# Kernel tuning notes

Measured on AMD Instinct MI355X. Metric: run time of the kernel, lower is better.

## Reference

```python
import jax, jax.numpy as jnp
import numpy as np

K = 10          # hardcoded in module (self.K = 10)
H = 26          # neighbors per query point in this run
PAD_H = 28      # layer_ind2neighbor[layer_ind=0]
KP_EXTENT = 1.2 # linear-influence extent


def setup_inputs() -> dict:
    key = jax.random.key(0)
    ks = jax.random.split(key, 6)
    N, Ns, Cin, Cout = 65536, 65536, 64, 128
    q_pts = jax.random.normal(ks[0], (N, 3), jnp.float32)
    s_pts = jax.random.normal(ks[1], (Ns, 3), jnp.float32)
    neighb_inds = jax.random.randint(ks[2], (N, H), 0, Ns)
    x = jax.random.normal(ks[3], (Ns, Cin), jnp.float32)
    # kernel_points_generator: Linear(PAD_H*3 -> K*3)
    gen_W = jax.random.normal(ks[4], (K * 3, PAD_H * 3), jnp.float32) * (1.0 / np.sqrt(PAD_H * 3))
    gen_b = jnp.zeros((K * 3,), jnp.float32)
    # KPConv weights: [K, in, out] (kaiming_uniform in torch; scaled normal here)
    weights = jax.random.normal(ks[5], (K, Cin, Cout), jnp.float32) * (1.0 / np.sqrt(Cin))
    return {"q_pts": q_pts, "s_pts": s_pts, "x": x,
            "gen_W": gen_W, "gen_b": gen_b, "weights": weights,
            "neighb_inds": neighb_inds}


def _kpconv(q_pts, s_pts, x, gen_W, gen_b, weights, neighb_inds):
    N = q_pts.shape[0]
    # shadow support point far away (index Ns)
    s_pad = jnp.concatenate([s_pts, jnp.full((1, 3), 1e6, s_pts.dtype)], axis=0)
    neighbors = s_pad[neighb_inds] - q_pts[:, None, :]                          # [N,H,3]
    # generative kernel points: pad neighbor list with -1 up to PAD_H, run linear
    padded = jnp.concatenate(
        [neighbors, jnp.full((N, PAD_H - H, 3), -1.0, neighbors.dtype)], axis=1)
    kp = (padded.reshape(N, -1) @ gen_W.T + gen_b).reshape(N, 1, K, 3)          # [N,1,K,3]
    diff = neighbors[:, :, None, :] - kp                                        # [N,H,K,3]
    sq_d = jnp.sum(diff * diff, axis=3)                                         # [N,H,K]
    # KP_influence == 'linear'
    all_w = jnp.maximum(1.0 - jnp.sqrt(sq_d) / KP_EXTENT, 0.0)
    all_w = jnp.swapaxes(all_w, 1, 2)                                           # [N,K,H]
    # shadow feature row (zeros) at index Ns
    x_pad = jnp.concatenate([x, jnp.zeros((1, x.shape[1]), x.dtype)], axis=0)
    neighb_x = x_pad[neighb_inds]                                               # [N,H,Cin]
    weighted = jnp.einsum('nkh,nhi->nki', all_w, neighb_x)                      # [N,K,Cin]
    return jnp.einsum('nki,kio->no', weighted, weights)                         # [N,Cout]


def reference(q_pts, s_pts, x, gen_W, gen_b, weights, neighb_inds):
    return _kpconv(q_pts, s_pts, x, gen_W, gen_b, weights, neighb_inds)
```

## Files before the change

kernel.cpp:

```cpp
#include <hip/hip_runtime.h>
#include <stdint.h>

#define N_Q   65536
#define N_S   65536
#define NB_H  26
#define PAD_H 28
#define KP    10
#define CIN   64
#define COUT  128
#define MT    8
#define BM    16
#define NPASS (BM / MT)

typedef unsigned short u16x8  __attribute__((ext_vector_type(8)));
typedef float          f32x4  __attribute__((ext_vector_type(4)));
typedef _Float16       f16x8  __attribute__((ext_vector_type(8)));
typedef _Float16       f16x2  __attribute__((ext_vector_type(2)));

#define CVT_BLOCKS 2049
#define PACK_BLOCKS 40

static __device__ __forceinline__ unsigned short f2h(float f) {
  return __builtin_bit_cast(unsigned short, (_Float16)f);
}

static __device__ __forceinline__ unsigned int pkrtz_u32(float a, float b) {
  return __builtin_bit_cast(unsigned int, __builtin_amdgcn_cvt_pkrtz(a, b));
}

static __device__ __forceinline__ float fdot2u(unsigned int a, unsigned int b, float c) {
#if __has_builtin(__builtin_amdgcn_fdot2)
  return __builtin_amdgcn_fdot2(__builtin_bit_cast(f16x2, a),
                                __builtin_bit_cast(f16x2, b), c, false);
#else
  f16x2 ha = __builtin_bit_cast(f16x2, a), hb = __builtin_bit_cast(f16x2, b);
  return c + (float)ha[0] * (float)hb[0] + (float)ha[1] * (float)hb[1];
#endif
}

__global__ void prep_kernel(const float* __restrict__ x,
                            const float* __restrict__ w,
                            unsigned short* __restrict__ xh,
                            unsigned short* __restrict__ bp) {
  if (blockIdx.x < CVT_BLOCKS) {
    long t = (long)blockIdx.x * blockDim.x + threadIdx.x;
    long off = t * 8;
    if (off >= (long)(N_S + 1) * CIN) return;
    u16x8 o;
    if (off < (long)N_S * CIN) {
      f32x4 a = *(const f32x4*)(x + off);
      f32x4 b = *(const f32x4*)(x + off + 4);
      o[0] = f2h(a[0]); o[1] = f2h(a[1]); o[2] = f2h(a[2]); o[3] = f2h(a[3]);
      o[4] = f2h(b[0]); o[5] = f2h(b[1]); o[6] = f2h(b[2]); o[7] = f2h(b[3]);
    } else {
      o = (u16x8)0;
    }
    *(u16x8*)(xh + off) = o;
  } else {
    int t = (blockIdx.x - CVT_BLOCKS) * blockDim.x + threadIdx.x;
    if (t >= 8 * 20 * 64) return;
    int lane = t & 63;
    int frag = t >> 6;
    int ks = frag % 20;
    int ct = frag / 20;
    int row0 = ks * 32 + (lane >> 4) * 8;
    int col  = ct * 16 + (lane & 15);
    u16x8 o;
    #pragma unroll
    for (int j = 0; j < 8; ++j) o[j] = f2h(w[(row0 + j) * COUT + col]);
    *(u16x8*)(bp + (long)t * 8) = o;
  }
}

__global__ void __launch_bounds__(256, 5)
kpconv_fused(const float* __restrict__ q_pts, const float* __restrict__ s_pts,
             const float* __restrict__ gen_W, const float* __restrict__ gen_b,
             const int* __restrict__ inds, const unsigned short* __restrict__ xh,
             const unsigned short* __restrict__ bp, float* __restrict__ out) {

  __shared__ int            sh_ind[MT][NB_H];
  __shared__ float          sh_nbr[MT][80];
  __shared__ float          sh_kp[MT][KP * 3];
  __shared__ unsigned int   sh_aw[MT][13][12];
  __shared__ unsigned short sA[20 * 512];

  const int  tid  = threadIdx.x;
  const long row0 = (long)blockIdx.x * BM;

  #pragma unroll 1
  for (int pass = 0; pass < NPASS; ++pass) {
    const int pbase = (int)row0 + pass * MT;

    if (tid < MT * NB_H) {
      int m = tid / NB_H, h = tid % NB_H;
      int n = pbase + m;
      int ind = inds[n * NB_H + h];
      sh_ind[m][h] = ind;
      float sx, sy, sz;
      if ((unsigned)ind < (unsigned)N_S) {
        sx = s_pts[ind * 3 + 0]; sy = s_pts[ind * 3 + 1]; sz = s_pts[ind * 3 + 2];
      } else {
        sx = 1e6f; sy = 1e6f; sz = 1e6f;
      }
      sh_nbr[m][h * 3 + 0] = sx - q_pts[n * 3 + 0];
      sh_nbr[m][h * 3 + 1] = sy - q_pts[n * 3 + 1];
      sh_nbr[m][h * 3 + 2] = sz - q_pts[n * 3 + 2];
    }
    if (tid < MT * 2) sh_nbr[tid >> 1][78 + (tid & 1)] = -1.0f;
    __syncthreads();

    if (tid < MT * KP * 3) {
      int m = tid / 30, r = tid % 30;
      const float* Wr = gen_W + r * (PAD_H * 3);
      const f32x4* W4 = (const f32x4*)Wr;
      const f32x4* N4 = (const f32x4*)&sh_nbr[m][0];
      f32x4 accv = {0.f, 0.f, 0.f, 0.f};
      #pragma unroll
      for (int j = 0; j < 20; ++j) accv += W4[j] * N4[j];
      sh_kp[m][r] = gen_b[r] - (Wr[80] + Wr[81] + Wr[82] + Wr[83])
                  + accv[0] + accv[1] + accv[2] + accv[3];
    }
    __syncthreads();

    for (int p = tid; p < MT * 13 * KP; p += 256) {
      int k = p % KP;
      int t = p / KP;
      int m = t & (MT - 1);
      int hp = t >> 3;
      float kx = sh_kp[m][k * 3 + 0], ky = sh_kp[m][k * 3 + 1], kz = sh_kp[m][k * 3 + 2];
      int h0 = hp * 2;
      float dx0 = sh_nbr[m][h0 * 3 + 0] - kx;
      float dy0 = sh_nbr[m][h0 * 3 + 1] - ky;
      float dz0 = sh_nbr[m][h0 * 3 + 2] - kz;
      float w0 = fmaxf(1.0f - sqrtf(dx0 * dx0 + dy0 * dy0 + dz0 * dz0) * (1.0f / 1.2f), 0.0f);
      float dx1 = sh_nbr[m][h0 * 3 + 3] - kx;
      float dy1 = sh_nbr[m][h0 * 3 + 4] - ky;
      float dz1 = sh_nbr[m][h0 * 3 + 5] - kz;
      float w1 = fmaxf(1.0f - sqrtf(dx1 * dx1 + dy1 * dy1 + dz1 * dz1) * (1.0f / 1.2f), 0.0f);
      sh_aw[m][hp][k] = pkrtz_u32(w0, w1);
    }
    __syncthreads();

    {
      const int m  = tid >> 5;
      const int i0 = (tid & 31) * 2;
      float acc0[KP], acc1[KP];
      #pragma unroll
      for (int k = 0; k < KP; ++k) { acc0[k] = 0.f; acc1[k] = 0.f; }

      unsigned int xr[8];
      #pragma unroll
      for (int h = 0; h < 8; ++h)
        xr[h] = *(const unsigned int*)(xh + (long)sh_ind[m][h] * CIN + i0);

      #pragma unroll
      for (int p = 0; p < 13; ++p) {
        unsigned int r0 = xr[(2 * p) & 7];
        unsigned int r1 = xr[(2 * p + 1) & 7];
        if (2 * p + 8 < NB_H)
          xr[(2 * p) & 7] = *(const unsigned int*)(xh + (long)sh_ind[m][2 * p + 8] * CIN + i0);
        if (2 * p + 9 < NB_H)
          xr[(2 * p + 1) & 7] = *(const unsigned int*)(xh + (long)sh_ind[m][2 * p + 9] * CIN + i0);
        unsigned int pair0 = __builtin_amdgcn_perm(r1, r0, 0x05040100u);
        unsigned int pair1 = __builtin_amdgcn_perm(r1, r0, 0x07060302u);
        const unsigned int* wrow = &sh_aw[m][p][0];
        #pragma unroll
        for (int k = 0; k < KP; ++k) {
          unsigned int w2 = wrow[k];
          acc0[k] = fdot2u(w2, pair0, acc0[k]);
          acc1[k] = fdot2u(w2, pair1, acc1[k]);
        }
      }
      const int row  = pass * MT + m;
      const int qhi  = i0 >> 5;
      const int e    = i0 & 31;
      const int slot = row * 4 + (e >> 3);
      const int hoff = slot * 8 + (e & 7);
      #pragma unroll
      for (int k = 0; k < KP; ++k)
        *(unsigned int*)(sA + (k * 2 + qhi) * 512 + hoff) = pkrtz_u32(acc0[k], acc1[k]);
    }
    __syncthreads();
  }

  {
    const int wave = tid >> 6;
    const int lane = tid & 63;
    const int ct0  = wave * 2, ct1 = ct0 + 1;
    const int aoff = ((lane & 15) * 4 + (lane >> 4)) * 8;

    f32x4 acc[2];
    acc[0] = (f32x4){0.f, 0.f, 0.f, 0.f};
    acc[1] = (f32x4){0.f, 0.f, 0.f, 0.f};

    u16x8 pb0[4], pb1[4];
    #pragma unroll
    for (int d = 0; d < 4; ++d) {
      pb0[d] = *(const u16x8*)(bp + (long)((ct0 * 20 + d) * 64 + lane) * 8);
      pb1[d] = *(const u16x8*)(bp + (long)((ct1 * 20 + d) * 64 + lane) * 8);
    }

    #pragma unroll
    for (int ks = 0; ks < 20; ++ks) {
      f16x8 b0 = __builtin_bit_cast(f16x8, pb0[ks & 3]);
      f16x8 b1 = __builtin_bit_cast(f16x8, pb1[ks & 3]);
      if (ks + 4 < 20) {
        pb0[ks & 3] = *(const u16x8*)(bp + (long)((ct0 * 20 + ks + 4) * 64 + lane) * 8);
        pb1[ks & 3] = *(const u16x8*)(bp + (long)((ct1 * 20 + ks + 4) * 64 + lane) * 8);
      }
      u16x8 au = *(const u16x8*)&sA[ks * 512 + aoff];
      f16x8 a = __builtin_bit_cast(f16x8, au);
      acc[0] = __builtin_amdgcn_mfma_f32_16x16x32_f16(a, b0, acc[0], 0, 0, 0);
      acc[1] = __builtin_amdgcn_mfma_f32_16x16x32_f16(a, b1, acc[1], 0, 0, 0);
    }

    const int col   = lane & 15;
    const int rbase = (lane >> 4) * 4;
    #pragma unroll
    for (int r = 0; r < 4; ++r) {
      long row = row0 + rbase + r;
      __builtin_nontemporal_store(acc[0][r], &out[row * COUT + ct0 * 16 + col]);
      __builtin_nontemporal_store(acc[1][r], &out[row * COUT + ct1 * 16 + col]);
    }
  }
}

extern "C" void kernel_launch(void* const* d_in, const int* in_sizes, int n_in,
                              void* d_out, int out_size, void* d_ws, size_t ws_size,
                              hipStream_t stream) {
  const float* q_pts = (const float*)d_in[0];
  const float* s_pts = (const float*)d_in[1];
  const float* x     = (const float*)d_in[2];
  const float* gen_W = (const float*)d_in[3];
  const float* gen_b = (const float*)d_in[4];
  const float* wts   = (const float*)d_in[5];
  const int*   inds  = (const int*)d_in[6];
  float* out = (float*)d_out;

  unsigned short* xh = (unsigned short*)d_ws;
  unsigned short* bp = xh + (size_t)(N_S + 1) * CIN;

  prep_kernel<<<CVT_BLOCKS + PACK_BLOCKS, 256, 0, stream>>>(x, wts, xh, bp);
  kpconv_fused<<<N_Q / BM, 256, 0, stream>>>(q_pts, s_pts, gen_W, gen_b,
                                             inds, xh, bp, out);
}
```

Before: 174.1 us.

## Process all 16 rows in one pass with two rows per thread and swizzled LDS

The two 8-row passes are merged into a single 16-row stage, so each thread gathers and accumulates features for two query rows (A and B) at once. This halves the number of block-wide barriers and doubles the independent gather loads in flight per thread. Kernel-weight reads from shared memory become vectorized 16/8-byte loads. The intermediate A-tile layout in shared memory is XOR-swizzled, with the MFMA-side address changed to match, to reduce bank conflicts. In exchange, register and LDS use per block rise, and launch bounds drop from 5 to 4 blocks per CU, lowering occupancy.

Result: no change. 175.7 us (+0.9%).

```diff
diff --git a/kernel.cpp b/kernel.cpp
--- a/kernel.cpp
+++ b/kernel.cpp
@@ -8,14 +8,15 @@
 #define KP    10
 #define CIN   64
 #define COUT  128
-#define MT    8
+#define MT    16
 #define BM    16
-#define NPASS (BM / MT)
 
 typedef unsigned short u16x8  __attribute__((ext_vector_type(8)));
 typedef float          f32x4  __attribute__((ext_vector_type(4)));
 typedef _Float16       f16x8  __attribute__((ext_vector_type(8)));
 typedef _Float16       f16x2  __attribute__((ext_vector_type(2)));
+typedef unsigned int   u32x4  __attribute__((ext_vector_type(4)));
+typedef unsigned int   u32x2  __attribute__((ext_vector_type(2)));
 
 #define CVT_BLOCKS 2049
 #define PACK_BLOCKS 40
@@ -72,7 +73,7 @@
   }
 }
 
-__global__ void __launch_bounds__(256, 5)
+__global__ void __launch_bounds__(256, 4)
 kpconv_fused(const float* __restrict__ q_pts, const float* __restrict__ s_pts,
              const float* __restrict__ gen_W, const float* __restrict__ gen_b,
              const int* __restrict__ inds, const unsigned short* __restrict__ xh,
@@ -87,107 +88,126 @@
   const int  tid  = threadIdx.x;
   const long row0 = (long)blockIdx.x * BM;
 
-  #pragma unroll 1
-  for (int pass = 0; pass < NPASS; ++pass) {
-    const int pbase = (int)row0 + pass * MT;
-
-    if (tid < MT * NB_H) {
-      int m = tid / NB_H, h = tid % NB_H;
-      int n = pbase + m;
-      int ind = inds[n * NB_H + h];
-      sh_ind[m][h] = ind;
-      float sx, sy, sz;
-      if ((unsigned)ind < (unsigned)N_S) {
-        sx = s_pts[ind * 3 + 0]; sy = s_pts[ind * 3 + 1]; sz = s_pts[ind * 3 + 2];
-      } else {
-        sx = 1e6f; sy = 1e6f; sz = 1e6f;
-      }
-      sh_nbr[m][h * 3 + 0] = sx - q_pts[n * 3 + 0];
-      sh_nbr[m][h * 3 + 1] = sy - q_pts[n * 3 + 1];
-      sh_nbr[m][h * 3 + 2] = sz - q_pts[n * 3 + 2];
-    }
-    if (tid < MT * 2) sh_nbr[tid >> 1][78 + (tid & 1)] = -1.0f;
-    __syncthreads();
-
-    if (tid < MT * KP * 3) {
-      int m = tid / 30, r = tid % 30;
-      const float* Wr = gen_W + r * (PAD_H * 3);
-      const f32x4* W4 = (const f32x4*)Wr;
-      const f32x4* N4 = (const f32x4*)&sh_nbr[m][0];
-      f32x4 accv = {0.f, 0.f, 0.f, 0.f};
+  for (int it = tid; it < MT * NB_H; it += 256) {
+    int m = it / NB_H, h = it % NB_H;
+    int n = (int)row0 + m;
+    int ind = inds[n * NB_H + h];
+    sh_ind[m][h] = ind;
+    float sx, sy, sz;
+    if ((unsigned)ind < (unsigned)N_S) {
+      sx = s_pts[ind * 3 + 0]; sy = s_pts[ind * 3 + 1]; sz = s_pts[ind * 3 + 2];
+    } else {
+      sx = 1e6f; sy = 1e6f; sz = 1e6f;
+    }
+    sh_nbr[m][h * 3 + 0] = sx - q_pts[n * 3 + 0];
+    sh_nbr[m][h * 3 + 1] = sy - q_pts[n * 3 + 1];
+    sh_nbr[m][h * 3 + 2] = sz - q_pts[n * 3 + 2];
+  }
+  if (tid < MT * 2) sh_nbr[tid >> 1][78 + (tid & 1)] = -1.0f;
+  __syncthreads();
+
+  for (int it = tid; it < MT * KP * 3; it += 256) {
+    int m = it / 30, r = it % 30;
+    const float* Wr = gen_W + r * (PAD_H * 3);
+    const f32x4* W4 = (const f32x4*)Wr;
+    const f32x4* N4 = (const f32x4*)&sh_nbr[m][0];
+    f32x4 accv = {0.f, 0.f, 0.f, 0.f};
+    #pragma unroll
+    for (int j = 0; j < 20; ++j) accv += W4[j] * N4[j];
+    sh_kp[m][r] = gen_b[r] - (Wr[80] + Wr[81] + Wr[82] + Wr[83])
+                + accv[0] + accv[1] + accv[2] + accv[3];
+  }
+  __syncthreads();
+
+  for (int p = tid; p < MT * 13 * KP; p += 256) {
+    int k = p % KP;
+    int t = p / KP;
+    int m = t & (MT - 1);
+    int hp = t >> 4;
+    float kx = sh_kp[m][k * 3 + 0], ky = sh_kp[m][k * 3 + 1], kz = sh_kp[m][k * 3 + 2];
+    int h0 = hp * 2;
+    float dx0 = sh_nbr[m][h0 * 3 + 0] - kx;
+    float dy0 = sh_nbr[m][h0 * 3 + 1] - ky;
+    float dz0 = sh_nbr[m][h0 * 3 + 2] - kz;
+    float w0 = fmaxf(1.0f - sqrtf(dx0 * dx0 + dy0 * dy0 + dz0 * dz0) * (1.0f / 1.2f), 0.0f);
+    float dx1 = sh_nbr[m][h0 * 3 + 3] - kx;
+    float dy1 = sh_nbr[m][h0 * 3 + 4] - ky;
+    float dz1 = sh_nbr[m][h0 * 3 + 5] - kz;
+    float w1 = fmaxf(1.0f - sqrtf(dx1 * dx1 + dy1 * dy1 + dz1 * dz1) * (1.0f / 1.2f), 0.0f);
+    sh_aw[m][hp][k] = pkrtz_u32(w0, w1);
+  }
+  __syncthreads();
+
+  {
+    const int g  = tid >> 5;
+    const int l  = tid & 31;
+    const int i0 = l * 2;
+    const int rA = g, rB = g + 8;
+
+    float a0A[KP], a1A[KP], a0B[KP], a1B[KP];
+    #pragma unroll
+    for (int k = 0; k < KP; ++k) { a0A[k] = 0.f; a1A[k] = 0.f; a0B[k] = 0.f; a1B[k] = 0.f; }
+
+    unsigned int xrA[8], xrB[8];
+    #pragma unroll
+    for (int h = 0; h < 8; ++h) {
+      xrA[h] = *(const unsigned int*)(xh + (long)sh_ind[rA][h] * CIN + i0);
+      xrB[h] = *(const unsigned int*)(xh + (long)sh_ind[rB][h] * CIN + i0);
+    }
+
+    #pragma unroll
+    for (int p = 0; p < 13; ++p) {
+      unsigned int r0A = xrA[(2 * p) & 7], r1A = xrA[(2 * p + 1) & 7];
+      unsigned int r0B = xrB[(2 * p) & 7], r1B = xrB[(2 * p + 1) & 7];
+      if (2 * p + 8 < NB_H) {
+        xrA[(2 * p) & 7] = *(const unsigned int*)(xh + (long)sh_ind[rA][2 * p + 8] * CIN + i0);
+        xrB[(2 * p) & 7] = *(const unsigned int*)(xh + (long)sh_ind[rB][2 * p + 8] * CIN + i0);
+      }
+      if (2 * p + 9 < NB_H) {
+        xrA[(2 * p + 1) & 7] = *(const unsigned int*)(xh + (long)sh_ind[rA][2 * p + 9] * CIN + i0);
+        xrB[(2 * p + 1) & 7] = *(const unsigned int*)(xh + (long)sh_ind[rB][2 * p + 9] * CIN + i0);
+      }
+      unsigned int p0A = __builtin_amdgcn_perm(r1A, r0A, 0x05040100u);
+      unsigned int p1A = __builtin_amdgcn_perm(r1A, r0A, 0x07060302u);
+      unsigned int p0B = __builtin_amdgcn_perm(r1B, r0B, 0x05040100u);
+      unsigned int p1B = __builtin_amdgcn_perm(r1B, r0B, 0x07060302u);
+
+      unsigned int wA[KP], wB[KP];
+      *(u32x4*)&wA[0] = *(const u32x4*)&sh_aw[rA][p][0];
+      *(u32x4*)&wA[4] = *(const u32x4*)&sh_aw[rA][p][4];
+      *(u32x2*)&wA[8] = *(const u32x2*)&sh_aw[rA][p][8];
+      *(u32x4*)&wB[0] = *(const u32x4*)&sh_aw[rB][p][0];
+      *(u32x4*)&wB[4] = *(const u32x4*)&sh_aw[rB][p][4];
+      *(u32x2*)&wB[8] = *(const u32x2*)&sh_aw[rB][p][8];
+
       #pragma unroll
-      for (int j = 0; j < 20; ++j) accv += W4[j] * N4[j];
-      sh_kp[m][r] = gen_b[r] - (Wr[80] + Wr[81] + Wr[82] + Wr[83])
-                  + accv[0] + accv[1] + accv[2] + accv[3];
-    }
-    __syncthreads();
-
-    for (int p = tid; p < MT * 13 * KP; p += 256) {
-      int k = p % KP;
-      int t = p / KP;
-      int m = t & (MT - 1);
-      int hp = t >> 3;
-      float kx = sh_kp[m][k * 3 + 0], ky = sh_kp[m][k * 3 + 1], kz = sh_kp[m][k * 3 + 2];
-      int h0 = hp * 2;
-      float dx0 = sh_nbr[m][h0 * 3 + 0] - kx;
-      float dy0 = sh_nbr[m][h0 * 3 + 1] - ky;
-      float dz0 = sh_nbr[m][h0 * 3 + 2] - kz;
-      float w0 = fmaxf(1.0f - sqrtf(dx0 * dx0 + dy0 * dy0 + dz0 * dz0) * (1.0f / 1.2f), 0.0f);
-      float dx1 = sh_nbr[m][h0 * 3 + 3] - kx;
-      float dy1 = sh_nbr[m][h0 * 3 + 4] - ky;
-      float dz1 = sh_nbr[m][h0 * 3 + 5] - kz;
-      float w1 = fmaxf(1.0f - sqrtf(dx1 * dx1 + dy1 * dy1 + dz1 * dz1) * (1.0f / 1.2f), 0.0f);
-      sh_aw[m][hp][k] = pkrtz_u32(w0, w1);
-    }
-    __syncthreads();
-
-    {
-      const int m  = tid >> 5;
-      const int i0 = (tid & 31) * 2;
-      float acc0[KP], acc1[KP];
-      #pragma unroll
-      for (int k = 0; k < KP; ++k) { acc0[k] = 0.f; acc1[k] = 0.f; }
-
-      unsigned int xr[8];
-      #pragma unroll
-      for (int h = 0; h < 8; ++h)
-        xr[h] = *(const unsigned int*)(xh + (long)sh_ind[m][h] * CIN + i0);
-
-      #pragma unroll
-      for (int p = 0; p < 13; ++p) {
-        unsigned int r0 = xr[(2 * p) & 7];
-        unsigned int r1 = xr[(2 * p + 1) & 7];
-        if (2 * p + 8 < NB_H)
-          xr[(2 * p) & 7] = *(const unsigned int*)(xh + (long)sh_ind[m][2 * p + 8] * CIN + i0);
-        if (2 * p + 9 < NB_H)
-          xr[(2 * p + 1) & 7] = *(const unsigned int*)(xh + (long)sh_ind[m][2 * p + 9] * CIN + i0);
-        unsigned int pair0 = __builtin_amdgcn_perm(r1, r0, 0x05040100u);
-        unsigned int pair1 = __builtin_amdgcn_perm(r1, r0, 0x07060302u);
-        const unsigned int* wrow = &sh_aw[m][p][0];
-        #pragma unroll
-        for (int k = 0; k < KP; ++k) {
-          unsigned int w2 = wrow[k];
-          acc0[k] = fdot2u(w2, pair0, acc0[k]);
-          acc1[k] = fdot2u(w2, pair1, acc1[k]);
-        }
-      }
-      const int row  = pass * MT + m;
-      const int qhi  = i0 >> 5;
-      const int e    = i0 & 31;
-      const int slot = row * 4 + (e >> 3);
-      const int hoff = slot * 8 + (e & 7);
-      #pragma unroll
-      for (int k = 0; k < KP; ++k)
-        *(unsigned int*)(sA + (k * 2 + qhi) * 512 + hoff) = pkrtz_u32(acc0[k], acc1[k]);
-    }
-    __syncthreads();
-  }
+      for (int k = 0; k < KP; ++k) {
+        a0A[k] = fdot2u(wA[k], p0A, a0A[k]);
+        a1A[k] = fdot2u(wA[k], p1A, a1A[k]);
+        a0B[k] = fdot2u(wB[k], p0B, a0B[k]);
+        a1B[k] = fdot2u(wB[k], p1B, a1B[k]);
+      }
+    }
+
+    const int kq  = (l & 15) >> 2;
+    const int qhi = l >> 4;
+    const int j2  = (2 * l) & 7;
+    const int swz = (kq << 3) ^ (qhi << 5);
+    const int hbA = (((kq * 16 + rA) * 8 + j2) ^ swz) + qhi * 512;
+    const int hbB = (((kq * 16 + rB) * 8 + j2) ^ swz) + qhi * 512;
+    #pragma unroll
+    for (int k = 0; k < KP; ++k) {
+      *(unsigned int*)(sA + k * 1024 + hbA) = pkrtz_u32(a0A[k], a1A[k]);
+      *(unsigned int*)(sA + k * 1024 + hbB) = pkrtz_u32(a0B[k], a1B[k]);
+    }
+  }
+  __syncthreads();
 
   {
     const int wave = tid >> 6;
     const int lane = tid & 63;
     const int ct0  = wave * 2, ct1 = ct0 + 1;
-    const int aoff = ((lane & 15) * 4 + (lane >> 4)) * 8;
+    const int a0   = (lane * 8) ^ ((lane >> 4) << 3);
 
     f32x4 acc[2];
     acc[0] = (f32x4){0.f, 0.f, 0.f, 0.f};
@@ -208,7 +228,7 @@
         pb0[ks & 3] = *(const u16x8*)(bp + (long)((ct0 * 20 + ks + 4) * 64 + lane) * 8);
         pb1[ks & 3] = *(const u16x8*)(bp + (long)((ct1 * 20 + ks + 4) * 64 + lane) * 8);
       }
-      u16x8 au = *(const u16x8*)&sA[ks * 512 + aoff];
+      u16x8 au = *(const u16x8*)&sA[ks * 512 + (a0 ^ ((ks & 1) << 5))];
       f16x8 a = __builtin_bit_cast(f16x8, au);
       acc[0] = __builtin_amdgcn_mfma_f32_16x16x32_f16(a, b0, acc[0], 0, 0, 0);
       acc[1] = __builtin_amdgcn_mfma_f32_16x16x32_f16(a, b1, acc[1], 0, 0, 0);
```
